# Kernel optimization log

Hardware: AMD Instinct MI355X
Metric: run time of the kernel (lower is better)

## Reference

```python
import jax, jax.numpy as jnp
import numpy as np


def setup_inputs() -> dict:
    key = jax.random.key(0)
    B, N = 32, 2048
    x = jax.random.normal(key, (B, N), dtype=jnp.float32)
    return {"input": x}


def reference(input) -> jnp.ndarray:
    # pair[b, i, j] = sigmoid(input[b, j] - input[b, i])  -> [B, N, N]
    pair = jax.nn.sigmoid(input[:, None, :] - input[:, :, None])
    # rr[b, i] = 1 / (sum_j pair[b, i, j] + 0.5)          -> [B, N]
    rr = 1.0 / (jnp.sum(pair, axis=-1) + 0.5)
    # loss uses only row 0 (positive doc's soft reciprocal rank)
    loss = -jnp.mean(rr[:, 0])
    return loss
```

## Files before the change

kernel.cpp:

```cpp
#include <hip/hip_runtime.h>


#define RL_B 32
#define RL_N 2048

__device__ __forceinline__ float sig(float d) {
    return 1.0f / (1.0f + __expf(-d));
}

__global__ __launch_bounds__(1024) void RankLoss_73959336837390_kernel(
    const float* __restrict__ x, float* __restrict__ out) {
    __shared__ float rr_s[RL_B];

    const int tid  = threadIdx.x;
    const int wave = tid >> 6;
    const int lane = tid & 63;

    const int b0 = wave;
    const int b1 = wave + 16;

    const float4* __restrict__ r0 = (const float4*)(x + b0 * RL_N);
    const float4* __restrict__ r1 = (const float4*)(x + b1 * RL_N);

    const float x0a = x[b0 * RL_N];
    const float x0b = x[b1 * RL_N];

    float4 va[8], vb[8];
    #pragma unroll
    for (int k = 0; k < 8; ++k) va[k] = r0[lane + (k << 6)];
    #pragma unroll
    for (int k = 0; k < 8; ++k) vb[k] = r1[lane + (k << 6)];

    float sa = 0.0f, sb = 0.0f;
    #pragma unroll
    for (int k = 0; k < 8; ++k) {
        sa += sig(va[k].x - x0a) + sig(va[k].y - x0a)
            + sig(va[k].z - x0a) + sig(va[k].w - x0a);
        sb += sig(vb[k].x - x0b) + sig(vb[k].y - x0b)
            + sig(vb[k].z - x0b) + sig(vb[k].w - x0b);
    }

    #pragma unroll
    for (int off = 32; off > 0; off >>= 1) {
        sa += __shfl_xor(sa, off, 64);
        sb += __shfl_xor(sb, off, 64);
    }

    if (lane == 0) {
        rr_s[b0] = 1.0f / (sa + 0.5f);
        rr_s[b1] = 1.0f / (sb + 0.5f);
    }

    __syncthreads();

    if (tid == 0) {
        float acc = 0.0f;
        #pragma unroll
        for (int b = 0; b < RL_B; ++b) acc += rr_s[b];
        *out = -acc / (float)RL_B;
    }
}

extern "C" void kernel_launch(void* const* d_in, const int* in_sizes, int n_in,
                              void* d_out, int out_size, void* d_ws, size_t ws_size,
                              hipStream_t stream) {
    const float* x = (const float*)d_in[0];
    float* out = (float*)d_out;
    RankLoss_73959336837390_kernel<<<1, 1024, 0, stream>>>(x, out);
}
```

Baseline: 60.80 us.

## Split row sums across 32 blocks with a separate reduce kernel

Replaces the single 1024-thread block that handled two rows per wave with 32 single-wave blocks, one per batch row, writing partial reciprocal ranks to the workspace. A second tiny kernel sums the 32 partials and writes the loss. This spreads the loads across many compute units instead of one, at the cost of an extra kernel launch and a global round trip for the partials.

```diff
diff --git a/kernel.cpp b/kernel.cpp
--- a/kernel.cpp
+++ b/kernel.cpp
@@ -8,63 +8,49 @@
     return 1.0f / (1.0f + __expf(-d));
 }
 
-__global__ __launch_bounds__(1024) void RankLoss_73959336837390_kernel(
-    const float* __restrict__ x, float* __restrict__ out) {
-    __shared__ float rr_s[RL_B];
+__global__ __launch_bounds__(64) void RankLoss_73959336837390_rows(
+    const float* __restrict__ x, float* __restrict__ partial) {
+    const int b    = blockIdx.x;
+    const int lane = threadIdx.x;
 
-    const int tid  = threadIdx.x;
-    const int wave = tid >> 6;
-    const int lane = tid & 63;
+    const float* __restrict__ row = x + b * RL_N;
+    const float4* __restrict__ r4 = (const float4*)row;
 
-    const int b0 = wave;
-    const int b1 = wave + 16;
+    const float x0 = row[0];
 
-    const float4* __restrict__ r0 = (const float4*)(x + b0 * RL_N);
-    const float4* __restrict__ r1 = (const float4*)(x + b1 * RL_N);
+    float4 v[8];
+    #pragma unroll
+    for (int k = 0; k < 8; ++k) v[k] = r4[lane + (k << 6)];
 
-    const float x0a = x[b0 * RL_N];
-    const float x0b = x[b1 * RL_N];
-
-    float4 va[8], vb[8];
-    #pragma unroll
-    for (int k = 0; k < 8; ++k) va[k] = r0[lane + (k << 6)];
-    #pragma unroll
-    for (int k = 0; k < 8; ++k) vb[k] = r1[lane + (k << 6)];
-
-    float sa = 0.0f, sb = 0.0f;
+    float s = 0.0f;
     #pragma unroll
     for (int k = 0; k < 8; ++k) {
-        sa += sig(va[k].x - x0a) + sig(va[k].y - x0a)
-            + sig(va[k].z - x0a) + sig(va[k].w - x0a);
-        sb += sig(vb[k].x - x0b) + sig(vb[k].y - x0b)
-            + sig(vb[k].z - x0b) + sig(vb[k].w - x0b);
+        s += sig(v[k].x - x0) + sig(v[k].y - x0)
+           + sig(v[k].z - x0) + sig(v[k].w - x0);
     }
 
     #pragma unroll
-    for (int off = 32; off > 0; off >>= 1) {
-        sa += __shfl_xor(sa, off, 64);
-        sb += __shfl_xor(sb, off, 64);
-    }
+    for (int off = 32; off > 0; off >>= 1) s += __shfl_xor(s, off, 64);
 
-    if (lane == 0) {
-        rr_s[b0] = 1.0f / (sa + 0.5f);
-        rr_s[b1] = 1.0f / (sb + 0.5f);
-    }
+    if (lane == 0) partial[b] = 1.0f / (s + 0.5f);
+}
 
-    __syncthreads();
-
-    if (tid == 0) {
-        float acc = 0.0f;
-        #pragma unroll
-        for (int b = 0; b < RL_B; ++b) acc += rr_s[b];
-        *out = -acc / (float)RL_B;
-    }
+__global__ __launch_bounds__(64) void RankLoss_73959336837390_reduce(
+    const float* __restrict__ partial, float* __restrict__ out) {
+    const int lane = threadIdx.x;
+    float v = (lane < RL_B) ? partial[lane] : 0.0f;
+    #pragma unroll
+    for (int off = 32; off > 0; off >>= 1) v += __shfl_xor(v, off, 64);
+    if (lane == 0) *out = -v / (float)RL_B;
 }
 
 extern "C" void kernel_launch(void* const* d_in, const int* in_sizes, int n_in,
                               void* d_out, int out_size, void* d_ws, size_t ws_size,
                               hipStream_t stream) {
     const float* x = (const float*)d_in[0];
-    float* out = (float*)d_out;
-    RankLoss_73959336837390_kernel<<<1, 1024, 0, stream>>>(x, out);
+    float* out     = (float*)d_out;
+    float* partial = (float*)d_ws;
+
+    RankLoss_73959336837390_rows<<<RL_B, 64, 0, stream>>>(x, partial);
+    RankLoss_73959336837390_reduce<<<1, 64, 0, stream>>>(partial, out);
 }
```

New measurement: 55.29 us, median of 2. 1.1x faster.
